# Kernel optimization log

Hardware: AMD Instinct MI355X
Metric: run time of the kernel (lower is better)

Reference implementation:

```python
import jax, jax.numpy as jnp
import numpy as np

B, C_FEAT, C_COND, C_KEY, H, W = 4, 256, 256, 32, 64, 64


def setup_inputs() -> dict:
    key = jax.random.key(0)
    ks = jax.random.split(key, 8)
    s = 0.02
    return {
        "features": jax.random.normal(ks[0], (B, C_FEAT, H, W), jnp.float32),
        "conditions": jax.random.normal(ks[1], (B, C_COND, H, W), jnp.float32),
        "Wq": jax.random.normal(ks[2], (C_KEY, C_COND), jnp.float32) * s,
        "bq": jnp.zeros((C_KEY,), jnp.float32),
        "Wk": jax.random.normal(ks[3], (C_KEY, C_FEAT), jnp.float32) * s,
        "bk": jnp.zeros((C_KEY,), jnp.float32),
        "Wv": jax.random.normal(ks[4], (C_FEAT, C_FEAT), jnp.float32) * s,
        "bv": jnp.zeros((C_FEAT,), jnp.float32),
        "gamma": jnp.zeros((1,), jnp.float32),
    }


def reference(features, conditions, Wq, bq, Wk, bk, Wv, bv, gamma):
    b, c, h, w = features.shape
    n = h * w
    feat = features.reshape(b, c, n)            # [B, C, N]
    cond = conditions.reshape(b, cond_c := conditions.shape[1], n)
    # 1x1 convs == per-pixel linear projections
    q = jnp.einsum('kc,bcn->bnk', Wq, cond) + bq          # [B, N, Ck]
    k = jnp.einsum('kc,bcn->bkn', Wk, feat) + bk[:, None]  # [B, Ck, N]
    v = jnp.einsum('oc,bcn->bon', Wv, feat) + bv[:, None]  # [B, C, N]
    energy = jnp.einsum('bik,bkj->bij', q, k)             # [B, N, N]
    attn = jax.nn.softmax(energy, axis=-1)
    out = jnp.einsum('bcj,bij->bci', v, attn)             # [B, C, N]
    out = out.reshape(b, c, h, w)
    return gamma * out + features
```

## Files before the change

kernel.cpp:

```cpp
#include <hip/hip_runtime.h>

typedef __bf16 bf16_t;
typedef __bf16 bf16x2 __attribute__((ext_vector_type(2)));
typedef __bf16 bf16x8 __attribute__((ext_vector_type(8)));
typedef float f32x4 __attribute__((ext_vector_type(4)));
typedef unsigned u32;
typedef unsigned u32x4 __attribute__((ext_vector_type(4)));

#define N_PIX 4096
#define CFEAT 256
#define CKEY 32
#define NBATCH 4

#if __has_builtin(__builtin_amdgcn_exp2f)
#define EXP2(x) __builtin_amdgcn_exp2f(x)
#else
#define EXP2(x) exp2f(x)
#endif

static __device__ __forceinline__ f32x4 mfma16(bf16x8 a, bf16x8 b, f32x4 c) {
    return __builtin_amdgcn_mfma_f32_16x16x32_bf16(a, b, c, 0, 0, 0);
}

static __device__ __forceinline__ void glds16(const void* g, void* l) {
    __builtin_amdgcn_global_load_lds(
        (const __attribute__((address_space(1))) void*)g,
        (__attribute__((address_space(3))) void*)l, 16, 0, 0);
}

static __device__ __forceinline__ u32 pk2(float lo, float hi) {
    bf16x2 t; t[0] = (bf16_t)lo; t[1] = (bf16_t)hi;
    return __builtin_bit_cast(u32, t);
}

static __device__ __forceinline__ void xpose4(u32 &x, u32 &y) {
#if __has_builtin(__builtin_amdgcn_permlane32_swap) && __has_builtin(__builtin_amdgcn_permlane16_swap)
    auto r32 = __builtin_amdgcn_permlane32_swap(x, y, false, false);
    auto r16 = __builtin_amdgcn_permlane16_swap(r32[0], r32[1], false, false);
    x = r16[0]; y = r16[1];
#else
    const int lane = threadIdx.x & 63;
    const int g = lane >> 4, ln = lane & 15;
    const int i0 = ln + ((g & 1) << 5);
    const int i2 = i0 + 16;
    u32 xs0 = (u32)__shfl((int)x, i0), ys0 = (u32)__shfl((int)y, i0);
    u32 xs2 = (u32)__shfl((int)x, i2), ys2 = (u32)__shfl((int)y, i2);
    x = (g < 2) ? xs0 : ys0;
    y = (g < 2) ? xs2 : ys2;
#endif
}

static __device__ __forceinline__ void softmax_tile(
    const bf16x8 kf[4], bf16x8 qf, bf16x8 ones,
    f32x4 &accsum, bf16x8 &pa0, bf16x8 &pa1)
{
    f32x4 zero = {0.f, 0.f, 0.f, 0.f};
    f32x4 st[4];
#pragma unroll
    for (int jt = 0; jt < 4; ++jt) st[jt] = mfma16(kf[jt], qf, zero);
    float ex[16];
#pragma unroll
    for (int jt = 0; jt < 4; ++jt)
#pragma unroll
        for (int r = 0; r < 4; ++r) ex[jt * 4 + r] = EXP2(st[jt][r]);
    u32 a0 = pk2(ex[0],  ex[1]),  a1 = pk2(ex[2],  ex[3]);
    u32 b0 = pk2(ex[4],  ex[5]),  b1 = pk2(ex[6],  ex[7]);
    u32 c0 = pk2(ex[8],  ex[9]),  c1 = pk2(ex[10], ex[11]);
    u32 d0 = pk2(ex[12], ex[13]), d1 = pk2(ex[14], ex[15]);
    xpose4(a0, b0); xpose4(a1, b1);
    xpose4(c0, d0); xpose4(c1, d1);
    u32x4 w0 = {a0, a1, b0, b1};
    u32x4 w1 = {c0, c1, d0, d1};
    pa0 = __builtin_bit_cast(bf16x8, w0);
    pa1 = __builtin_bit_cast(bf16x8, w1);
    accsum = mfma16(ones, pa0, accsum);
    accsum = mfma16(ones, pa1, accsum);
}

__global__ __launch_bounds__(256) void proj_kernel(
    const float* __restrict__ Wq, const float* __restrict__ bq, const float* __restrict__ cond,
    const float* __restrict__ Wk, const float* __restrict__ bk, const float* __restrict__ feat,
    const float* __restrict__ Wv, const float* __restrict__ bv,
    bf16_t* __restrict__ Qt, bf16_t* __restrict__ Kt, bf16_t* __restrict__ Vv)
{
    __shared__ __attribute__((aligned(16))) bf16_t T[64][40];
    const int lane = threadIdx.x & 63, wave = threadIdx.x >> 6;
    const int g = lane >> 4, ln = lane & 15;
    const int bid = blockIdx.x;
    f32x4 zero = {0.f, 0.f, 0.f, 0.f};

    if (bid < 512) {
        const bool isK = (bid >= 256);
        const int idx = bid & 255;
        const int xt = idx & 63;
        const int b  = idx >> 6;
        const float* W    = isK ? Wk : Wq;
        const float* bias = isK ? bk : bq;
        const float* X  = (isK ? feat : cond) + (size_t)b * CFEAT * N_PIX;
        bf16_t*      Yt = (isK ? Kt : Qt) + (size_t)b * N_PIX * CKEY;
        const float qscale = isK ? 1.0f : 1.4426950408889634f;

        const int m_base = (wave & 1) * 16;
        const int n_loc  = (wave >> 1) * 32;
        const int n_base = xt * 64 + n_loc;

        f32x4 acc[2] = {zero, zero};
        for (int k0 = 0; k0 < CFEAT; k0 += 32) {
            bf16x8 a;
            const float* wp = W + (size_t)(m_base + ln) * CFEAT + k0 + g * 8;
#pragma unroll
            for (int j = 0; j < 8; ++j) a[j] = (bf16_t)wp[j];
#pragma unroll
            for (int nt = 0; nt < 2; ++nt) {
                const float* xp = X + (size_t)(k0 + g * 8) * N_PIX + n_base + nt * 16 + ln;
                bf16x8 bfr;
#pragma unroll
                for (int j = 0; j < 8; ++j) bfr[j] = (bf16_t)xp[(size_t)j * N_PIX];
                acc[nt] = mfma16(a, bfr, acc[nt]);
            }
        }
#pragma unroll
        for (int nt = 0; nt < 2; ++nt)
#pragma unroll
            for (int r = 0; r < 4; ++r) {
                const int ck = m_base + g * 4 + r;
                T[n_loc + nt * 16 + ln][ck] = (bf16_t)((acc[nt][r] + bias[ck]) * qscale);
            }
        __syncthreads();
        const int n  = threadIdx.x >> 2;
        const int sg = threadIdx.x & 3;
        bf16x8 row = *(const bf16x8*)&T[n][sg * 8];
        *(bf16x8*)&Yt[(size_t)(xt * 64 + n) * CKEY + sg * 8] = row;
    } else {
        const int idx = bid - 512;
        const int xt = idx & 127;
        const int b  = idx >> 7;
        const int n_base = xt * 32;
        const int c_wave = wave * 64;
        const float* Xb = feat + (size_t)b * CFEAT * N_PIX;
        bf16_t*      Vb = Vv + (size_t)b * CFEAT * N_PIX;

        f32x4 acc[4][2];
#pragma unroll
        for (int mt = 0; mt < 4; ++mt) { acc[mt][0] = zero; acc[mt][1] = zero; }

        for (int k0 = 0; k0 < CFEAT; k0 += 32) {
            bf16x8 bfr[2];
#pragma unroll
            for (int nt = 0; nt < 2; ++nt) {
                const float* xp = Xb + (size_t)(k0 + g * 8) * N_PIX + n_base + nt * 16 + ln;
#pragma unroll
                for (int j = 0; j < 8; ++j) bfr[nt][j] = (bf16_t)xp[(size_t)j * N_PIX];
            }
#pragma unroll
            for (int mt = 0; mt < 4; ++mt) {
                const float* wp = Wv + (size_t)(c_wave + mt * 16 + ln) * CFEAT + k0 + g * 8;
                bf16x8 a;
#pragma unroll
                for (int j = 0; j < 8; ++j) a[j] = (bf16_t)wp[j];
                acc[mt][0] = mfma16(a, bfr[0], acc[mt][0]);
                acc[mt][1] = mfma16(a, bfr[1], acc[mt][1]);
            }
        }
#pragma unroll
        for (int mt = 0; mt < 4; ++mt)
#pragma unroll
            for (int nt = 0; nt < 2; ++nt)
#pragma unroll
                for (int r = 0; r < 4; ++r) {
                    const int m = c_wave + mt * 16 + g * 4 + r;
                    const int n = n_base + nt * 16 + ln;
                    Vb[(size_t)m * N_PIX + n] = (bf16_t)(acc[mt][nt][r] + bv[m]);
                }
    }
}

__global__ __launch_bounds__(256, 2) void pv_kernel(
    const bf16_t* __restrict__ Qt, const bf16_t* __restrict__ Kt,
    const bf16_t* __restrict__ V,
    const float* __restrict__ features, const float* __restrict__ gamma,
    float* __restrict__ out)
{
    __shared__ __attribute__((aligned(16))) bf16_t Vlds[2][16384];
    __shared__ __attribute__((aligned(16))) bf16_t Plds[2][2048];
    __shared__ float Llds[32];

    const int lane = threadIdx.x & 63, wave = threadIdx.x >> 6;
    const int g = lane >> 4, ln = lane & 15;
    const int f = blockIdx.x;
    const int b = (f & 7) >> 1;
    const int i_tile = (f & 1) + 2 * (f >> 3);
    const int i_base = i_tile * 32;
    const bool sm = (wave < 2);

    const bf16_t* Qb = Qt + (size_t)b * N_PIX * CKEY;
    const bf16_t* Kb = Kt + (size_t)b * N_PIX * CKEY;
    const bf16_t* Vb = V + (size_t)b * CFEAT * N_PIX;

    const int nq = sm ? 4 : 12;
    const int sbase = sm ? (wave * 64 + lane) : (512 + (wave - 2) * 64 + lane);
    const bf16_t* vgp[12];
#pragma unroll
    for (int q = 0; q < 12; ++q) {
        const int s = sbase + (q < nq ? q : 0) * 128;
        const int sc = s >> 3, sj = (s & 7) ^ (sc & 7);
        vgp[q] = Vb + (size_t)sc * N_PIX + sj * 8;
    }

#define STAGE(BUF, JOFF)                                                      \
    if (sm) {                                                                 \
        _Pragma("unroll") for (int q = 0; q < 4; ++q)                         \
            glds16(vgp[q] + (JOFF), &Vlds[BUF][(sbase + q * 128) * 8]);       \
    } else {                                                                  \
        _Pragma("unroll") for (int q = 0; q < 12; ++q)                        \
            glds16(vgp[q] + (JOFF), &Vlds[BUF][(sbase + q * 128) * 8]);       \
    }

#define LOADK(DST, JQ)                                                        \
    { _Pragma("unroll") for (int jt = 0; jt < 4; ++jt)                        \
        DST[jt] = *(const bf16x8*)&Kb[(size_t)((JQ) + jt * 16 + ln) * CKEY + g * 8]; }

#define PWRITE(SLOT, PA0, PA1)                                                \
    { const int ir = wave * 16 + ln;                                          \
      char* Pw = (char*)&Plds[SLOT][0] + ir * 128;                            \
      *(bf16x8*)(Pw + ((g)     ^ (ir & 7)) * 16) = PA0;                       \
      *(bf16x8*)(Pw + ((4 + g) ^ (ir & 7)) * 16) = PA1; }

    bf16x8 qf = {};
    if (sm) qf = *(const bf16x8*)&Qb[(size_t)(i_base + wave * 16 + ln) * CKEY + g * 8];

    bf16x8 ones;
#pragma unroll
    for (int j = 0; j < 8; ++j) ones[j] = (bf16_t)1.0f;

    f32x4 zero = {0.f, 0.f, 0.f, 0.f};
    f32x4 acc[4][2];
#pragma unroll
    for (int ct = 0; ct < 4; ++ct) { acc[ct][0] = zero; acc[ct][1] = zero; }
    f32x4 accsum = zero;

    bf16x8 kfA[4], kfB[4];

    {
        bf16x8 kf0[4];
        if (sm) LOADK(kf0, 0);
        asm volatile("" ::: "memory");
        STAGE(0, 0);
        if (sm) {
            bf16x8 pa0, pa1;
            softmax_tile(kf0, qf, ones, accsum, pa0, pa1);
            PWRITE(0, pa0, pa1);
            LOADK(kfA, 64);
        }
        asm volatile("s_waitcnt vmcnt(0)" ::: "memory");
        asm volatile("s_waitcnt lgkmcnt(0)" ::: "memory");
        __builtin_amdgcn_s_barrier();
        asm volatile("" ::: "memory");
    }

#define PV_ITER(NN, KU, KN)                                                   \
  {                                                                           \
    const int nn = (NN);                                                      \
    const bf16_t* Vt = &Vlds[nn & 1][0];                                      \
    bf16x8 vf[8];                                                             \
    _Pragma("unroll")                                                         \
    for (int ct = 0; ct < 4; ++ct)                                            \
      _Pragma("unroll")                                                       \
      for (int s = 0; s < 2; ++s) {                                           \
        const int c = wave * 64 + ct * 16 + ln;                               \
        vf[ct * 2 + s] = *(const bf16x8*)&Vt[(c * 8 + ((s * 4 + g) ^ (c & 7))) * 8]; \
      }                                                                       \
    const char* Pr = (const char*)&Plds[nn & 1][0];                           \
    bf16x8 pf[4];                                                             \
    _Pragma("unroll")                                                         \
    for (int it = 0; it < 2; ++it)                                            \
      _Pragma("unroll")                                                       \
      for (int s = 0; s < 2; ++s)                                             \
        pf[it * 2 + s] = *(const bf16x8*)(Pr + (it * 16 + ln) * 128           \
                           + ((s * 4 + g) ^ (ln & 7)) * 16);                  \
    STAGE((nn + 1) & 1, (((nn + 1) & 63) * 64));                              \
    const bool live = (nn < 63);                                              \
    if (sm && live) {                                                         \
      LOADK(KN, ((nn + 2) & 63) * 64);                                        \
      bf16x8 pa0, pa1;                                                        \
      softmax_tile(KU, qf, ones, accsum, pa0, pa1);                           \
      PWRITE((nn + 1) & 1, pa0, pa1);                                         \
    }                                                                         \
    if (sm) { asm volatile("s_waitcnt vmcnt(4)" ::: "memory"); }              \
    else    { asm volatile("s_waitcnt vmcnt(0)" ::: "memory"); }              \
    asm volatile("s_waitcnt lgkmcnt(0)" ::: "memory");                        \
    __builtin_amdgcn_s_barrier();                                             \
    asm volatile("" ::: "memory");                                            \
    __builtin_amdgcn_s_setprio(1);                                            \
    _Pragma("unroll")                                                         \
    for (int ct = 0; ct < 4; ++ct)                                            \
      _Pragma("unroll")                                                       \
      for (int it = 0; it < 2; ++it) {                                        \
        acc[ct][it] = mfma16(vf[ct * 2 + 0], pf[it * 2 + 0], acc[ct][it]);    \
        acc[ct][it] = mfma16(vf[ct * 2 + 1], pf[it * 2 + 1], acc[ct][it]);    \
      }                                                                       \
    __builtin_amdgcn_s_setprio(0);                                            \
  }

    for (int n2 = 0; n2 < 32; ++n2) {
        PV_ITER(2 * n2,     kfA, kfB);
        PV_ITER(2 * n2 + 1, kfB, kfA);
    }
#undef PV_ITER

    if (sm && g == 0) Llds[wave * 16 + ln] = accsum[0];
    __syncthreads();
    const float gam = gamma[0];
    float sc2[2];
#pragma unroll
    for (int it = 0; it < 2; ++it) sc2[it] = gam / Llds[it * 16 + ln];

#pragma unroll
    for (int ct = 0; ct < 4; ++ct)
#pragma unroll
        for (int it = 0; it < 2; ++it)
#pragma unroll
            for (int r = 0; r < 4; ++r) {
                const int c = wave * 64 + ct * 16 + g * 4 + r;
                const int i = i_base + it * 16 + ln;
                const size_t idx = ((size_t)b * CFEAT + c) * N_PIX + i;
                out[idx] = sc2[it] * acc[ct][it][r] + features[idx];
            }
#undef STAGE
#undef LOADK
#undef PWRITE
}

extern "C" void kernel_launch(void* const* d_in, const int* in_sizes, int n_in,
                              void* d_out, int out_size, void* d_ws, size_t ws_size,
                              hipStream_t stream) {
    const float* features   = (const float*)d_in[0];
    const float* conditions = (const float*)d_in[1];
    const float* Wq  = (const float*)d_in[2];
    const float* bq  = (const float*)d_in[3];
    const float* Wk  = (const float*)d_in[4];
    const float* bk  = (const float*)d_in[5];
    const float* Wv  = (const float*)d_in[6];
    const float* bv  = (const float*)d_in[7];
    const float* gam = (const float*)d_in[8];
    float* out = (float*)d_out;

    bf16_t* Qt = (bf16_t*)d_ws;
    bf16_t* Kt = Qt + (size_t)NBATCH * N_PIX * CKEY;
    bf16_t* Vw = Kt + (size_t)NBATCH * N_PIX * CKEY;

    proj_kernel<<<dim3(1024, 1, 1), 256, 0, stream>>>(
        Wq, bq, conditions, Wk, bk, features, Wv, bv, Qt, Kt, Vw);
    pv_kernel<<<dim3(512, 1, 1), 256, 0, stream>>>(
        Qt, Kt, Vw, features, gam, out);
}
```

Before: 173.0 us.

## Load V fragments directly into registers instead of staging through LDS

Removes the 64KB double-buffered V LDS staging via global_load_lds and has each wave load its own V MFMA fragments straight from global memory into double-buffered registers. It also rotates which waves compute the softmax tiles depending on block parity. The aim is to cut LDS capacity and traffic and the vmcnt waits, which may allow more occupancy. In exchange, register pressure goes up, global loads become strided across rows with no cooperative coalescing, and the explicit vmcnt waits are replaced by whatever the compiler inserts.

```diff
diff --git a/kernel.cpp b/kernel.cpp
--- a/kernel.cpp
+++ b/kernel.cpp
@@ -20,12 +20,6 @@
 
 static __device__ __forceinline__ f32x4 mfma16(bf16x8 a, bf16x8 b, f32x4 c) {
     return __builtin_amdgcn_mfma_f32_16x16x32_bf16(a, b, c, 0, 0, 0);
-}
-
-static __device__ __forceinline__ void glds16(const void* g, void* l) {
-    __builtin_amdgcn_global_load_lds(
-        (const __attribute__((address_space(1))) void*)g,
-        (__attribute__((address_space(3))) void*)l, 16, 0, 0);
 }
 
 static __device__ __forceinline__ u32 pk2(float lo, float hi) {
@@ -181,7 +175,6 @@
     const float* __restrict__ features, const float* __restrict__ gamma,
     float* __restrict__ out)
 {
-    __shared__ __attribute__((aligned(16))) bf16_t Vlds[2][16384];
     __shared__ __attribute__((aligned(16))) bf16_t Plds[2][2048];
     __shared__ float Llds[32];
 
@@ -191,43 +184,38 @@
     const int b = (f & 7) >> 1;
     const int i_tile = (f & 1) + 2 * (f >> 3);
     const int i_base = i_tile * 32;
-    const bool sm = (wave < 2);
+    const int rw = wave ^ ((f & 1) << 1);
+    const bool sm = (rw < 2);
+    const int sw = rw & 1;
 
     const bf16_t* Qb = Qt + (size_t)b * N_PIX * CKEY;
     const bf16_t* Kb = Kt + (size_t)b * N_PIX * CKEY;
     const bf16_t* Vb = V + (size_t)b * CFEAT * N_PIX;
 
-    const int nq = sm ? 4 : 12;
-    const int sbase = sm ? (wave * 64 + lane) : (512 + (wave - 2) * 64 + lane);
-    const bf16_t* vgp[12];
-#pragma unroll
-    for (int q = 0; q < 12; ++q) {
-        const int s = sbase + (q < nq ? q : 0) * 128;
-        const int sc = s >> 3, sj = (s & 7) ^ (sc & 7);
-        vgp[q] = Vb + (size_t)sc * N_PIX + sj * 8;
-    }
-
-#define STAGE(BUF, JOFF)                                                      \
-    if (sm) {                                                                 \
-        _Pragma("unroll") for (int q = 0; q < 4; ++q)                         \
-            glds16(vgp[q] + (JOFF), &Vlds[BUF][(sbase + q * 128) * 8]);       \
-    } else {                                                                  \
-        _Pragma("unroll") for (int q = 0; q < 12; ++q)                        \
-            glds16(vgp[q] + (JOFF), &Vlds[BUF][(sbase + q * 128) * 8]);       \
-    }
+    const bf16_t* vbase[8];
+#pragma unroll
+    for (int ct = 0; ct < 4; ++ct)
+#pragma unroll
+        for (int s = 0; s < 2; ++s)
+            vbase[ct * 2 + s] = Vb + (size_t)(wave * 64 + ct * 16 + ln) * N_PIX
+                                   + (s * 4 + g) * 8;
+
+#define LOADV(DST, JO)                                                        \
+    { _Pragma("unroll") for (int q = 0; q < 8; ++q)                           \
+        DST[q] = *(const bf16x8*)(vbase[q] + (JO)); }
 
 #define LOADK(DST, JQ)                                                        \
     { _Pragma("unroll") for (int jt = 0; jt < 4; ++jt)                        \
         DST[jt] = *(const bf16x8*)&Kb[(size_t)((JQ) + jt * 16 + ln) * CKEY + g * 8]; }
 
 #define PWRITE(SLOT, PA0, PA1)                                                \
-    { const int ir = wave * 16 + ln;                                          \
+    { const int ir = sw * 16 + ln;                                            \
       char* Pw = (char*)&Plds[SLOT][0] + ir * 128;                            \
       *(bf16x8*)(Pw + ((g)     ^ (ir & 7)) * 16) = PA0;                       \
       *(bf16x8*)(Pw + ((4 + g) ^ (ir & 7)) * 16) = PA1; }
 
     bf16x8 qf = {};
-    if (sm) qf = *(const bf16x8*)&Qb[(size_t)(i_base + wave * 16 + ln) * CKEY + g * 8];
+    if (sm) qf = *(const bf16x8*)&Qb[(size_t)(i_base + sw * 16 + ln) * CKEY + g * 8];
 
     bf16x8 ones;
 #pragma unroll
@@ -240,36 +228,26 @@
     f32x4 accsum = zero;
 
     bf16x8 kfA[4], kfB[4];
+    bf16x8 vfA[8], vfB[8];
 
     {
         bf16x8 kf0[4];
         if (sm) LOADK(kf0, 0);
-        asm volatile("" ::: "memory");
-        STAGE(0, 0);
+        LOADV(vfA, 0);
         if (sm) {
             bf16x8 pa0, pa1;
             softmax_tile(kf0, qf, ones, accsum, pa0, pa1);
             PWRITE(0, pa0, pa1);
             LOADK(kfA, 64);
         }
-        asm volatile("s_waitcnt vmcnt(0)" ::: "memory");
         asm volatile("s_waitcnt lgkmcnt(0)" ::: "memory");
         __builtin_amdgcn_s_barrier();
         asm volatile("" ::: "memory");
     }
 
-#define PV_ITER(NN, KU, KN)                                                   \
+#define PV_ITER(NN, VU, VN, KU, KN)                                           \
   {                                                                           \
     const int nn = (NN);                                                      \
-    const bf16_t* Vt = &Vlds[nn & 1][0];                                      \
-    bf16x8 vf[8];                                                             \
-    _Pragma("unroll")                                                         \
-    for (int ct = 0; ct < 4; ++ct)                                            \
-      _Pragma("unroll")                                                       \
-      for (int s = 0; s < 2; ++s) {                                           \
-        const int c = wave * 64 + ct * 16 + ln;                               \
-        vf[ct * 2 + s] = *(const bf16x8*)&Vt[(c * 8 + ((s * 4 + g) ^ (c & 7))) * 8]; \
-      }                                                                       \
     const char* Pr = (const char*)&Plds[nn & 1][0];                           \
     bf16x8 pf[4];                                                             \
     _Pragma("unroll")                                                         \
@@ -278,7 +256,7 @@
       for (int s = 0; s < 2; ++s)                                             \
         pf[it * 2 + s] = *(const bf16x8*)(Pr + (it * 16 + ln) * 128           \
                            + ((s * 4 + g) ^ (ln & 7)) * 16);                  \
-    STAGE((nn + 1) & 1, (((nn + 1) & 63) * 64));                              \
+    LOADV(VN, (((nn + 1) & 63) * 64));                                        \
     const bool live = (nn < 63);                                              \
     if (sm && live) {                                                         \
       LOADK(KN, ((nn + 2) & 63) * 64);                                        \
@@ -286,8 +264,6 @@
       softmax_tile(KU, qf, ones, accsum, pa0, pa1);                           \
       PWRITE((nn + 1) & 1, pa0, pa1);                                         \
     }                                                                         \
-    if (sm) { asm volatile("s_waitcnt vmcnt(4)" ::: "memory"); }              \
-    else    { asm volatile("s_waitcnt vmcnt(0)" ::: "memory"); }              \
     asm volatile("s_waitcnt lgkmcnt(0)" ::: "memory");                        \
     __builtin_amdgcn_s_barrier();                                             \
     asm volatile("" ::: "memory");                                            \
@@ -296,19 +272,19 @@
     for (int ct = 0; ct < 4; ++ct)                                            \
       _Pragma("unroll")                                                       \
       for (int it = 0; it < 2; ++it) {                                        \
-        acc[ct][it] = mfma16(vf[ct * 2 + 0], pf[it * 2 + 0], acc[ct][it]);    \
-        acc[ct][it] = mfma16(vf[ct * 2 + 1], pf[it * 2 + 1], acc[ct][it]);    \
+        acc[ct][it] = mfma16(VU[ct * 2 + 0], pf[it * 2 + 0], acc[ct][it]);    \
+        acc[ct][it] = mfma16(VU[ct * 2 + 1], pf[it * 2 + 1], acc[ct][it]);    \
       }                                                                       \
     __builtin_amdgcn_s_setprio(0);                                            \
   }
 
     for (int n2 = 0; n2 < 32; ++n2) {
-        PV_ITER(2 * n2,     kfA, kfB);
-        PV_ITER(2 * n2 + 1, kfB, kfA);
+        PV_ITER(2 * n2,     vfA, vfB, kfA, kfB);
+        PV_ITER(2 * n2 + 1, vfB, vfA, kfB, kfA);
     }
 #undef PV_ITER
 
-    if (sm && g == 0) Llds[wave * 16 + ln] = accsum[0];
+    if (sm && g == 0) Llds[sw * 16 + ln] = accsum[0];
     __syncthreads();
     const float gam = gamma[0];
     float sc2[2];
@@ -326,7 +302,7 @@
                 const size_t idx = ((size_t)b * CFEAT + c) * N_PIX + i;
                 out[idx] = sc2[it] * acc[ct][it][r] + features[idx];
             }
-#undef STAGE
+#undef LOADV
 #undef LOADK
 #undef PWRITE
 }
```

Result: slower. 243.9 us (+41.0%).
